# Kernel optimization log

Hardware: AMD Instinct MI355X
Metric: run time of the kernel (lower is better)

## Reference

```python
import jax, jax.numpy as jnp
from jax import lax
import numpy as np

H = 32  # hidden_size

def setup_inputs() -> dict:
    key = jax.random.key(0)
    ks = jax.random.split(key, 7)
    B, T = 32, 16384
    s = 1.0 / np.sqrt(H)  # torch LSTM/Linear init scale
    x = jax.random.normal(ks[0], (B, T, 1), dtype=jnp.float32)
    W_ih = jax.random.uniform(ks[1], (4 * H, 1), jnp.float32, -s, s)
    W_hh = jax.random.uniform(ks[2], (4 * H, H), jnp.float32, -s, s)
    b_ih = jax.random.uniform(ks[3], (4 * H,), jnp.float32, -s, s)
    b_hh = jax.random.uniform(ks[4], (4 * H,), jnp.float32, -s, s)
    W_out = jax.random.uniform(ks[5], (1, H), jnp.float32, -s, s)
    b_out = jax.random.uniform(ks[6], (1,), jnp.float32, -s, s)
    return {"x": x, "W_ih": W_ih, "W_hh": W_hh, "b_ih": b_ih,
            "b_hh": b_hh, "W_out": W_out, "b_out": b_out}

def reference(x, W_ih, W_hh, b_ih, b_hh, W_out, b_out):
    B, T, _ = x.shape
    # Precompute input contribution to all gates once: (B, T, 4H)
    pre = jnp.einsum('bti,gi->btg', x, W_ih) + b_ih + b_hh

    def step(carry, p_t):
        h, c = carry
        gates = p_t + h @ W_hh.T  # (B, 4H), torch gate order i,f,g,o
        i, f, g, o = jnp.split(gates, 4, axis=-1)
        c = jax.nn.sigmoid(f) * c + jax.nn.sigmoid(i) * jnp.tanh(g)
        h = jax.nn.sigmoid(o) * jnp.tanh(c)
        return (h, c), h

    h0 = jnp.zeros((B, H), x.dtype)
    (_, _), hs = lax.scan(step, (h0, h0), jnp.swapaxes(pre, 0, 1))
    hs = jnp.swapaxes(hs, 0, 1)  # (B, T, H)
    return hs @ W_out.T + b_out  # (B, T, 1)
```

## Files before the change

kernel.cpp:

```cpp
#include <hip/hip_runtime.h>

#define T_LEN 16384
#define BATCH 32
#define HID 32
#define L2E 1.44269504088896340736f
#define SCLG (-2.0f * 1.44269504088896340736f)

typedef float f2 __attribute__((ext_vector_type(2)));
typedef unsigned u2_t __attribute__((ext_vector_type(2)));

#if __has_builtin(__builtin_amdgcn_exp2f)
#define EXP2F(x) __builtin_amdgcn_exp2f(x)
#else
#define EXP2F(x) __exp2f(x)
#endif
#if __has_builtin(__builtin_amdgcn_rcpf)
#define RCPF(x) __builtin_amdgcn_rcpf(x)
#else
#define RCPF(x) (1.0f / (x))
#endif

__device__ __forceinline__ float rlane(float v, int lane) {
    return __int_as_float(__builtin_amdgcn_readlane(__float_as_int(v), lane));
}

__device__ __forceinline__ float xhalf_lo_to_hi(float v) {
#if __has_builtin(__builtin_amdgcn_permlane32_swap)
    u2_t r = __builtin_amdgcn_permlane32_swap(__float_as_uint(v), __float_as_uint(v),
                                              false, false);
    return __uint_as_float(r.x);
#else
    return __shfl_xor(v, 32, 64);
#endif
}

__global__ __launch_bounds__(64) __attribute__((amdgpu_waves_per_eu(1, 1)))
void lstm_seq_kernel(const float* __restrict__ x,
                     const float* __restrict__ W_ih,
                     const float* __restrict__ W_hh,
                     const float* __restrict__ b_ih,
                     const float* __restrict__ b_hh,
                     const float* __restrict__ W_out,
                     const float* __restrict__ b_out,
                     float* __restrict__ out)
{
    const int b    = blockIdx.x;
    const int lane = threadIdx.x;
    const int j    = lane & 31;
    const bool upper = (lane >= 32);

    const int rowA = upper ? (32 + j) : j;
    const int rowB = upper ? (96 + j) : (64 + j);

    const float sclA = -L2E;
    const float sclB = upper ? -L2E : SCLG;

    f2 Wa2[16], Wb2[16];
    const f2* ra2 = reinterpret_cast<const f2*>(W_hh + (size_t)rowA * HID);
    const f2* rb2 = reinterpret_cast<const f2*>(W_hh + (size_t)rowB * HID);
    #pragma unroll
    for (int q = 0; q < 16; ++q) { Wa2[q] = ra2[q] * sclA; Wb2[q] = rb2[q] * sclB; }
    #pragma unroll
    for (int q = 0; q < 16; ++q) { asm("" : "+v"(Wa2[q]), "+v"(Wb2[q])); }

    const float wihA = sclA * W_ih[rowA];
    const float wihB = sclB * W_ih[rowB];
    const float bA = sclA * (b_ih[rowA] + b_hh[rowA]);
    const float bB = sclB * (b_ih[rowB] + b_hh[rowB]);

    const float wout = W_out[j];
    const float bout = b_out[0];

    __shared__ float phist[64 * 65];
    __shared__ float hbuf[64];

    float cS = 0.0f;
    hbuf[lane] = 0.0f;
    __syncthreads();

    const float* xb = x + (size_t)b * T_LEN;
    float*       yb = out + (size_t)b * T_LEN;
    const f2* hb2 = reinterpret_cast<const f2*>(&hbuf[32]);

    float xv = xb[lane];

    for (int t0 = 0; t0 < T_LEN; t0 += 64) {
        float xv_next = (t0 + 64 < T_LEN) ? xb[t0 + 64 + lane] : 0.0f;

        #pragma unroll 4
        for (int s = 0; s < 64; ++s) {
            const float xs  = rlane(xv, s);
            const float xpA = fmaf(xs, wihA, bA);
            const float xpB = fmaf(xs, wihB, bB);

            f2 hv2[16];
            #pragma unroll
            for (int p = 0; p < 16; ++p) hv2[p] = hb2[p];

            f2 zA[4], zB[4];
            zA[0].x = xpA; zA[0].y = 0.0f;
            zB[0].x = xpB; zB[0].y = 0.0f;
            #pragma unroll
            for (int p = 0; p < 16; ++p) {
                if (p == 0) {
                    asm("v_pk_fma_f32 %0, %1, %2, %0"
                        : "+v"(zA[0]) : "v"(hv2[0]), "v"(Wa2[0]));
                    asm("v_pk_fma_f32 %0, %1, %2, %0"
                        : "+v"(zB[0]) : "v"(hv2[0]), "v"(Wb2[0]));
                } else if (p < 4) {
                    asm("v_pk_mul_f32 %0, %1, %2"
                        : "=v"(zA[p]) : "v"(hv2[p]), "v"(Wa2[p]));
                    asm("v_pk_mul_f32 %0, %1, %2"
                        : "=v"(zB[p]) : "v"(hv2[p]), "v"(Wb2[p]));
                } else {
                    asm("v_pk_fma_f32 %0, %1, %2, %0"
                        : "+v"(zA[p & 3]) : "v"(hv2[p]), "v"(Wa2[p]));
                    asm("v_pk_fma_f32 %0, %1, %2, %0"
                        : "+v"(zB[p & 3]) : "v"(hv2[p]), "v"(Wb2[p]));
                }
            }
            const f2 rA = (zA[0] + zA[1]) + (zA[2] + zA[3]);
            const f2 rB = (zB[0] + zB[1]) + (zB[2] + zB[3]);
            const float za = rA.x + rA.y;
            const float zb = rB.x + rB.y;

            const float A = RCPF(1.0f + EXP2F(za));
            const float r = RCPF(1.0f + EXP2F(zb));
            const float tgS = fmaf(r, 2.0f * SCLG, -SCLG);
            const float so2 = r + r;

            const float up = A * tgS;
            const float tu = xhalf_lo_to_hi(up);

            cS = fmaf(A, cS, tu);
            const float r2 = RCPF(1.0f + EXP2F(cS));
            const float h  = fmaf(so2, r2, -r);

            hbuf[lane] = h;
            phist[s * 65 + lane] = h * wout;
        }

        __syncthreads();
        float acc = bout;
        #pragma unroll
        for (int k = 0; k < HID; ++k) acc += phist[lane * 65 + 32 + k];
        yb[t0 + lane] = acc;
        __syncthreads();

        xv = xv_next;
    }
}

extern "C" void kernel_launch(void* const* d_in, const int* in_sizes, int n_in,
                              void* d_out, int out_size, void* d_ws, size_t ws_size,
                              hipStream_t stream) {
    const float* x     = (const float*)d_in[0];
    const float* W_ih  = (const float*)d_in[1];
    const float* W_hh  = (const float*)d_in[2];
    const float* b_ih  = (const float*)d_in[3];
    const float* b_hh  = (const float*)d_in[4];
    const float* W_out = (const float*)d_in[5];
    const float* b_out = (const float*)d_in[6];
    float* out = (float*)d_out;

    lstm_seq_kernel<<<BATCH, 64, 0, stream>>>(x, W_ih, W_hh, b_ih, b_hh,
                                              W_out, b_out, out);
}
```

Measured before the change: 3.066 ms.

## Broadcast hidden state via readlane into SGPRs instead of LDS round-trip

Replaces the per-step LDS write/read of the hidden state with 32 v_readlane operations that place h into scalar registers, which then feed the packed FMAs directly as SGPR operands. The aim is to take LDS store-to-load latency off the serial recurrence critical path. The cost is 32 readlanes per step, with possible VALU-to-SGPR hazard stalls, and packed FMA may be restricted in how many SGPR operands it accepts. It also splits the output reduction into four accumulators to shorten that dependency chain.

```diff
diff --git a/kernel.cpp b/kernel.cpp
--- a/kernel.cpp
+++ b/kernel.cpp
@@ -72,15 +72,15 @@
     const float bout = b_out[0];
 
     __shared__ float phist[64 * 65];
-    __shared__ float hbuf[64];
 
     float cS = 0.0f;
-    hbuf[lane] = 0.0f;
-    __syncthreads();
+
+    f2 hp[16];
+    #pragma unroll
+    for (int p = 0; p < 16; ++p) hp[p] = (f2){0.0f, 0.0f};
 
     const float* xb = x + (size_t)b * T_LEN;
     float*       yb = out + (size_t)b * T_LEN;
-    const f2* hb2 = reinterpret_cast<const f2*>(&hbuf[32]);
 
     float xv = xb[lane];
 
@@ -93,10 +93,6 @@
             const float xpA = fmaf(xs, wihA, bA);
             const float xpB = fmaf(xs, wihB, bB);
 
-            f2 hv2[16];
-            #pragma unroll
-            for (int p = 0; p < 16; ++p) hv2[p] = hb2[p];
-
             f2 zA[4], zB[4];
             zA[0].x = xpA; zA[0].y = 0.0f;
             zB[0].x = xpB; zB[0].y = 0.0f;
@@ -104,19 +100,19 @@
             for (int p = 0; p < 16; ++p) {
                 if (p == 0) {
                     asm("v_pk_fma_f32 %0, %1, %2, %0"
-                        : "+v"(zA[0]) : "v"(hv2[0]), "v"(Wa2[0]));
+                        : "+v"(zA[0]) : "s"(hp[0]), "v"(Wa2[0]));
                     asm("v_pk_fma_f32 %0, %1, %2, %0"
-                        : "+v"(zB[0]) : "v"(hv2[0]), "v"(Wb2[0]));
+                        : "+v"(zB[0]) : "s"(hp[0]), "v"(Wb2[0]));
                 } else if (p < 4) {
                     asm("v_pk_mul_f32 %0, %1, %2"
-                        : "=v"(zA[p]) : "v"(hv2[p]), "v"(Wa2[p]));
+                        : "=v"(zA[p]) : "s"(hp[p]), "v"(Wa2[p]));
                     asm("v_pk_mul_f32 %0, %1, %2"
-                        : "=v"(zB[p]) : "v"(hv2[p]), "v"(Wb2[p]));
+                        : "=v"(zB[p]) : "s"(hp[p]), "v"(Wb2[p]));
                 } else {
                     asm("v_pk_fma_f32 %0, %1, %2, %0"
-                        : "+v"(zA[p & 3]) : "v"(hv2[p]), "v"(Wa2[p]));
+                        : "+v"(zA[p & 3]) : "s"(hp[p]), "v"(Wa2[p]));
                     asm("v_pk_fma_f32 %0, %1, %2, %0"
-                        : "+v"(zB[p & 3]) : "v"(hv2[p]), "v"(Wb2[p]));
+                        : "+v"(zB[p & 3]) : "s"(hp[p]), "v"(Wb2[p]));
                 }
             }
             const f2 rA = (zA[0] + zA[1]) + (zA[2] + zA[3]);
@@ -136,15 +132,27 @@
             const float r2 = RCPF(1.0f + EXP2F(cS));
             const float h  = fmaf(so2, r2, -r);
 
-            hbuf[lane] = h;
+            #pragma unroll
+            for (int p = 0; p < 16; ++p) {
+                f2 t;
+                t.x = rlane(h, 32 + 2 * p);
+                t.y = rlane(h, 33 + 2 * p);
+                hp[p] = t;
+            }
+
             phist[s * 65 + lane] = h * wout;
         }
 
         __syncthreads();
-        float acc = bout;
+        float a0 = bout, a1 = 0.0f, a2 = 0.0f, a3 = 0.0f;
         #pragma unroll
-        for (int k = 0; k < HID; ++k) acc += phist[lane * 65 + 32 + k];
-        yb[t0 + lane] = acc;
+        for (int k = 0; k < HID; k += 4) {
+            a0 += phist[lane * 65 + 32 + k];
+            a1 += phist[lane * 65 + 33 + k];
+            a2 += phist[lane * 65 + 34 + k];
+            a3 += phist[lane * 65 + 35 + k];
+        }
+        yb[t0 + lane] = (a0 + a1) + (a2 + a3);
         __syncthreads();
 
         xv = xv_next;
```

Result: slower. 3.545 ms (+15.6%).
